# Kernel optimization log

Hardware: AMD Instinct MI355X
Metric: run time of the kernel (lower is better)

Reference implementation:

```python
import jax, jax.numpy as jnp
import numpy as np

# ---- quantization scales (per-tensor, as produced by from_float calibration) ----
IN_SCALE = 0.05      # ForwardTokenizer: fp32 hidden -> int8
ALPHA_Q = 1e-4       # W8A8B8O8 requant multipliers (already include 1/sqrt(head_dim) for q)
ALPHA_K = 1e-4
ALPHA_V = 1e-4
QK_ALPHA = 1e-3      # BMM_S8T_S8N_F32T dequant scale (q_scale * k_scale)
PV_ALPHA = 1.0/127.0 # BMM_S8T_S8N_S8T requant scale ((1/127)*v_scale/out_scale)
OUT_ALPHA = 1e-4     # W8A8BFP32OFP32 dequant scale
NUM_HEADS = 32


def _quant_i8(x, scale):
    # simulate int8 quantization in fp32 (values are exact small integers)
    return jnp.clip(jnp.round(x / scale), -128.0, 127.0)


def _w8a8b8o8(x_i8, W_i8, b_i8, alpha):
    # int8 GEMM with int8 bias, requantized to int8: clamp(round(alpha*(x@W^T) + b))
    acc = jnp.einsum('btd,ed->bte', x_i8, W_i8)  # int32 accumulator in fp32
    return jnp.clip(jnp.round(alpha * acc + b_i8), -128.0, 127.0)


def setup_inputs() -> dict:
    key = jax.random.key(0)
    ks = jax.random.split(key, 10)
    B, T, D = 2, 2048, 2560
    hidden_states = jax.random.normal(ks[0], (B, T, D), dtype=jnp.float32)
    # causal additive mask, shape (B,1,T,T)
    neg = jnp.float32(-1e9)
    causal = jnp.where(jnp.tril(jnp.ones((T, T), dtype=bool)), 0.0, neg)
    attention_mask = jnp.broadcast_to(causal[None, None], (B, 1, T, T)).astype(jnp.float32)
    # int8-valued weights/biases stored as fp32 integers in [-127,127]
    def i8(k, shape):
        return jax.random.randint(k, shape, -127, 128).astype(jnp.float32)
    Wq = i8(ks[1], (D, D)); bq = i8(ks[2], (D,))
    Wk = i8(ks[3], (D, D)); bk = i8(ks[4], (D,))
    Wv = i8(ks[5], (D, D)); bv = i8(ks[6], (D,))
    Wo = i8(ks[7], (D, D))
    bo = jax.random.normal(ks[8], (D,), dtype=jnp.float32) * 0.01  # fp32 out bias
    return {"hidden_states": hidden_states, "attention_mask": attention_mask,
            "Wq": Wq, "bq": bq, "Wk": Wk, "bk": bk, "Wv": Wv, "bv": bv,
            "Wo": Wo, "bo": bo}


def reference(hidden_states, attention_mask, Wq, bq, Wk, bk, Wv, bv, Wo, bo):
    B, T, D = hidden_states.shape
    H = NUM_HEADS
    Dh = D // H
    # ForwardTokenizer: fp32 -> int8
    x_i8 = _quant_i8(hidden_states, IN_SCALE)
    # fused int8 q/k/v projections (W8A8B8O8Linear)
    q = _w8a8b8o8(x_i8, Wq, bq, ALPHA_Q)
    k = _w8a8b8o8(x_i8, Wk, bk, ALPHA_K)
    v = _w8a8b8o8(x_i8, Wv, bv, ALPHA_V)
    # (B,T,D) -> (B,H,T,Dh)
    def shape(t):
        return t.reshape(B, T, H, Dh).transpose(0, 2, 1, 3)
    q, k, v = shape(q), shape(k), shape(v)
    # BMM_S8T_S8N_F32T: int8 q @ k^T dequantized to fp32
    attn_weights = QK_ALPHA * jnp.einsum('bhqd,bhkd->bhqk', q, k)
    attn_weights = attn_weights + attention_mask  # (B,H,T,T)
    attn_weights = jnp.maximum(attn_weights, jnp.finfo(jnp.float32).min)
    attn_probs = jax.nn.softmax(attn_weights, axis=-1)
    # requantize probs to int8: mul_(127).round_()
    p_i8 = jnp.round(attn_probs * 127.0)
    # BMM_S8T_S8N_S8T: int8 p @ v requantized to int8
    attn_out = jnp.clip(jnp.round(PV_ALPHA * jnp.einsum('bhqk,bhkd->bhqd', p_i8, v)), -128.0, 127.0)
    # (B,H,T,Dh) -> (B,T,D)
    attn_out = attn_out.transpose(0, 2, 1, 3).reshape(B, T, D)
    # W8A8BFP32OFP32Linear: int8 GEMM, fp32 dequant + fp32 bias
    out = OUT_ALPHA * jnp.einsum('btd,ed->bte', attn_out, Wo) + bo
    return out
```

## Files before the change

### kernel.cpp

```cpp
#include <hip/hip_runtime.h>
#include <stdint.h>

typedef int v4i __attribute__((ext_vector_type(4)));

#define MFMA_I8(a,b,c) __builtin_amdgcn_mfma_i32_16x16x64_i8(a,b,c,0,0,0)

#define TD 2560
#define TT 2048
#define TB 2
#define TH 32
#define TDH 80
#define TDHP 128
#define TM 4096

#define LOG2E_MS 1.4426950408889634e-3f
#define MASKI (-(1<<30))
#define MAGICF 12582912.0f

__device__ __forceinline__ float clamp8f(float v){ return fminf(fmaxf(v, -128.0f), 127.0f); }
__device__ __forceinline__ float fexp2(float x){ return __builtin_amdgcn_exp2f(x); }

__device__ __forceinline__ void gl_lds16(const int8_t* g, int8_t* l){
  __builtin_amdgcn_global_load_lds(
      (const __attribute__((address_space(1))) void*)g,
      (__attribute__((address_space(3))) void*)l, 16, 0, 0);
}

__global__ void k_quant(const float* __restrict__ x, int8_t* __restrict__ y, int n4){
  int stride = gridDim.x * blockDim.x;
  for (int i = blockIdx.x*blockDim.x + threadIdx.x; i < n4; i += stride){
    float4 v = ((const float4*)x)[i];
    char4 o;
    o.x = (int8_t)clamp8f(rintf(__fdiv_rn(v.x, 0.05f)));
    o.y = (int8_t)clamp8f(rintf(__fdiv_rn(v.y, 0.05f)));
    o.z = (int8_t)clamp8f(rintf(__fdiv_rn(v.z, 0.05f)));
    o.w = (int8_t)clamp8f(rintf(__fdiv_rn(v.w, 0.05f)));
    ((char4*)y)[i] = o;
  }
}

__global__ void k_conv4(const float* __restrict__ w0, const float* __restrict__ w1,
                        const float* __restrict__ w2, const float* __restrict__ w3,
                        int8_t* __restrict__ y0, int8_t* __restrict__ y1,
                        int8_t* __restrict__ y2, int8_t* __restrict__ y3, int n4){
  const int z = blockIdx.y;
  const float* w = z == 0 ? w0 : (z == 1 ? w1 : (z == 2 ? w2 : w3));
  int8_t* y = z == 0 ? y0 : (z == 1 ? y1 : (z == 2 ? y2 : y3));
  int stride = gridDim.x * blockDim.x;
  for (int i = blockIdx.x*blockDim.x + threadIdx.x; i < n4; i += stride){
    float4 v = ((const float4*)w)[i];
    char4 o;
    o.x = (int8_t)(int)rintf(v.x);
    o.y = (int8_t)(int)rintf(v.y);
    o.z = (int8_t)(int)rintf(v.z);
    o.w = (int8_t)(int)rintf(v.w);
    ((char4*)y)[i] = o;
  }
}

#define GB_SETUP                                                     \
  const int t = threadIdx.x;                                         \
  const int wv = t >> 6, l = t & 63, lhi = (l >> 4) & 3, llo = l & 15;\
  const int wr = wv >> 1, wc = wv & 1;                               \
  const int grow = t >> 3;                                           \
  const int gcol = ((t & 7) ^ ((t >> 3) & 7)) * 16;                  \
  const int sc0 = ((lhi ^ (llo & 7)) << 4);

#define GB_KLOOP(xsrc, wsrc)                                         \
  const int8_t* xa = (xsrc) + (size_t)(m0 + grow)*TD + gcol;         \
  const int8_t* wb = (wsrc) + (size_t)(n0 + grow)*TD + gcol;         \
  v4i acc[4][4] = {};                                                \
  for (int k0 = 0; k0 < TD; k0 += 128){                              \
    _Pragma("unroll")                                                \
    for (int i = 0; i < 4; ++i){                                     \
      gl_lds16(xa + (size_t)(i*32)*TD + k0, &As[(i*32 + wv*8)*128]); \
      gl_lds16(wb + (size_t)(i*32)*TD + k0, &Bs[(i*32 + wv*8)*128]); \
    }                                                                \
    __syncthreads();                                                 \
    v4i a[4][2], b[4][2];                                            \
    _Pragma("unroll")                                                \
    for (int mi = 0; mi < 4; ++mi){                                  \
      a[mi][0] = *(const v4i*)&As[(wr*64 + mi*16 + llo)*128 + sc0];  \
      a[mi][1] = *(const v4i*)&As[(wr*64 + mi*16 + llo)*128 + (sc0 ^ 64)];\
    }                                                                \
    _Pragma("unroll")                                                \
    for (int ni = 0; ni < 4; ++ni){                                  \
      b[ni][0] = *(const v4i*)&Bs[(wc*64 + ni*16 + llo)*128 + sc0];  \
      b[ni][1] = *(const v4i*)&Bs[(wc*64 + ni*16 + llo)*128 + (sc0 ^ 64)];\
    }                                                                \
    _Pragma("unroll")                                                \
    for (int mi = 0; mi < 4; ++mi)                                   \
      _Pragma("unroll")                                              \
      for (int ni = 0; ni < 4; ++ni){                                \
        acc[mi][ni] = MFMA_I8(a[mi][0], b[ni][0], acc[mi][ni]);      \
        acc[mi][ni] = MFMA_I8(a[mi][1], b[ni][1], acc[mi][ni]);      \
      }                                                              \
    __syncthreads();                                                 \
  }

__global__ __launch_bounds__(256) void k_qkvg(const int8_t* __restrict__ x,
    const int8_t* __restrict__ w0_, const int8_t* __restrict__ w1_, const int8_t* __restrict__ w2_,
    const float* __restrict__ b0_, const float* __restrict__ b1_, const float* __restrict__ b2_,
    int8_t* __restrict__ dq, int8_t* __restrict__ dk, int8_t* __restrict__ dv)
{
  __shared__ __align__(16) int8_t As[128*128];
  __shared__ __align__(16) int8_t Bs[128*128];
  const int z = blockIdx.z;
  const int8_t* w = z == 0 ? w0_ : (z == 1 ? w1_ : w2_);
  const float* bias = z == 0 ? b0_ : (z == 1 ? b1_ : b2_);
  const int m0 = blockIdx.x * 128, n0 = blockIdx.y * 128;
  GB_SETUP;
  GB_KLOOP(x, w);

  #pragma unroll
  for (int mi = 0; mi < 4; ++mi)
  #pragma unroll
  for (int ni = 0; ni < 4; ++ni)
  #pragma unroll
  for (int r = 0; r < 4; ++r){
    int rowg = m0 + wr*64 + mi*16 + lhi*4 + r;
    int colg = n0 + wc*64 + ni*16 + llo;
    float fv = __fadd_rn(__fmul_rn(1e-4f, (float)acc[mi][ni][r]), bias[colg]);
    int8_t q8 = (int8_t)clamp8f(rintf(fv));
    int bb = rowg >> 11, tl = rowg & 2047;
    int hh = colg / 80, dh = colg - hh*80;
    if (z == 0)      dq[((size_t)(bb*TH + hh)*TT + tl)*TDHP + dh] = q8;
    else if (z == 1) dk[((size_t)(bb*TH + hh)*TT + tl)*TDHP + dh] = q8;
    else             dv[((size_t)(bb*TH + hh)*TDH + dh)*TT + tl] = q8;
  }
}

__global__ __launch_bounds__(256) void k_oproj128(const int8_t* __restrict__ x,
    const int8_t* __restrict__ w, const float* __restrict__ bo,
    float* __restrict__ out)
{
  __shared__ __align__(16) int8_t As[128*128];
  __shared__ __align__(16) int8_t Bs[128*128];
  const int m0 = blockIdx.x * 128, n0 = blockIdx.y * 128;
  GB_SETUP;
  GB_KLOOP(x, w);

  #pragma unroll
  for (int mi = 0; mi < 4; ++mi)
  #pragma unroll
  for (int ni = 0; ni < 4; ++ni)
  #pragma unroll
  for (int r = 0; r < 4; ++r){
    int rowg = m0 + wr*64 + mi*16 + lhi*4 + r;
    int colg = n0 + wc*64 + ni*16 + llo;
    out[(size_t)rowg*TD + colg] =
        __fadd_rn(__fmul_rn(1e-4f, (float)acc[mi][ni][r]), bo[colg]);
  }
}

__global__ __launch_bounds__(256, 6) void k_attn6(const int8_t* __restrict__ qb_,
    const int8_t* __restrict__ kb_, const int8_t* __restrict__ vt_,
    int8_t* __restrict__ ao)
{
  __shared__ __align__(16) int8_t Ks[64*128];
  const int flat = blockIdx.x;
  const int g = flat & 7, ii = flat >> 3;
  const int qt = 31 - (ii >> 3);
  const int pair = g*8 + (ii & 7);
  const int h = pair & 31, b = pair >> 5;

  const int t = threadIdx.x, wv = t >> 6, l = t & 63, lhi = (l >> 4) & 3, llo = l & 15;
  const size_t bh = (size_t)(b*TH + h);
  const int8_t* qb = qb_ + bh*TT*TDHP;
  const int8_t* kb = kb_ + bh*TT*TDHP;
  const int8_t* vb = vt_ + bh*TDH*TT;

  const int qw0 = qt*64 + wv*16;
  const int qg = qw0 + llo;
  const int ktmax = qt + 1;

  int koff0[4], koff1[4];
  #pragma unroll
  for (int sub = 0; sub < 4; ++sub){
    const int row = sub*16 + llo, sw = row & 7;
    koff0[sub] = row*128 + (((lhi  ) ^ sw) << 4);
    koff1[sub] = row*128 + (((lhi+4) ^ sw) << 4);
  }

  v4i qa0 = *(const v4i*)(qb + (size_t)(qw0 + llo)*TDHP + lhi*16);
  v4i qa1 = {0,0,0,0};
  if (lhi == 0) qa1 = *(const v4i*)(qb + (size_t)(qw0 + llo)*TDHP + 64);

  const int srow = t >> 2, scp = (t & 3) * 2, ssw = srow & 7;
  const int8_t* kg = kb + (size_t)srow*TDHP + scp*16;
  int8_t* sdst0 = &Ks[srow*128 + (((scp  ) ^ ssw) << 4)];
  int8_t* sdst1 = &Ks[srow*128 + (((scp+1) ^ ssw) << 4)];

  int   M  = MASKI;
  float cm = __fmul_rn(LOG2E_MS, (float)MASKI);
  float ls = 0.0f;

  v4i pr0 = *(const v4i*)(kg);
  v4i pr1 = *(const v4i*)(kg + 16);
  *(v4i*)sdst0 = pr0; *(v4i*)sdst1 = pr1;
  for (int kt = 0; kt < ktmax; ++kt){
    if (kt + 1 < ktmax){
      pr0 = *(const v4i*)(kg + (size_t)(kt+1)*64*TDHP);
      pr1 = *(const v4i*)(kg + (size_t)(kt+1)*64*TDHP + 16);
    }
    __syncthreads();
    int sv[4][4];
    if (kt < qt){
      #pragma unroll
      for (int sub = 0; sub < 4; ++sub){
        v4i kf0 = *(const v4i*)&Ks[koff0[sub]];
        v4i kf1 = *(const v4i*)&Ks[koff1[sub]];
        v4i d = {}; d = MFMA_I8(kf0, qa0, d); d = MFMA_I8(kf1, qa1, d);
        sv[sub][0]=d[0]; sv[sub][1]=d[1]; sv[sub][2]=d[2]; sv[sub][3]=d[3];
      }
    } else {
      #pragma unroll
      for (int sub = 0; sub < 4; ++sub){
        if (sub <= wv){
          v4i kf0 = *(const v4i*)&Ks[koff0[sub]];
          v4i kf1 = *(const v4i*)&Ks[koff1[sub]];
          v4i d = {}; d = MFMA_I8(kf0, qa0, d); d = MFMA_I8(kf1, qa1, d);
          const int base = kt*64 + sub*16 + lhi*4;
          #pragma unroll
          for (int r = 0; r < 4; ++r)
            sv[sub][r] = (base + r <= qg) ? d[r] : MASKI;
        } else {
          #pragma unroll
          for (int r = 0; r < 4; ++r) sv[sub][r] = MASKI;
        }
      }
    }
    int m0 = max(max(sv[0][0], sv[0][1]), sv[0][2]);
    int m1 = max(max(sv[0][3], sv[1][0]), sv[1][1]);
    int m2 = max(max(sv[1][2], sv[1][3]), sv[2][0]);
    int m3 = max(max(sv[2][1], sv[2][2]), sv[2][3]);
    int m4 = max(max(sv[3][0], sv[3][1]), sv[3][2]);
    int tm = max(max(max(m0, m1), max(m2, m3)), max(m4, sv[3][3]));
    int Mn = max(M, tm);
    float cmN = __fmul_rn(LOG2E_MS, (float)Mn);
    float fac = fexp2(__fsub_rn(cm, cmN));
    float tot = 0.0f;
    #pragma unroll
    for (int sub = 0; sub < 4; ++sub){
      float e0 = fexp2(__fmaf_rn((float)sv[sub][0], LOG2E_MS, -cmN));
      float e1 = fexp2(__fmaf_rn((float)sv[sub][1], LOG2E_MS, -cmN));
      float e2 = fexp2(__fmaf_rn((float)sv[sub][2], LOG2E_MS, -cmN));
      float e3 = fexp2(__fmaf_rn((float)sv[sub][3], LOG2E_MS, -cmN));
      tot = __fadd_rn(tot, __fadd_rn(__fadd_rn(e0, e1), __fadd_rn(e2, e3)));
    }
    ls = __fmaf_rn(ls, fac, tot);
    M = Mn; cm = cmN;
    __syncthreads();
    if (kt + 1 < ktmax){ *(v4i*)sdst0 = pr0; *(v4i*)sdst1 = pr1; }
  }

  float rq;
  {
    float mm = cm, ll = ls;
    #pragma unroll
    for (int off = 16; off < 64; off <<= 1){
      float om = __shfl_xor(mm, off);
      float ol = __shfl_xor(ll, off);
      float mn = fmaxf(mm, om);
      ll = __fadd_rn(__fmul_rn(ll, fexp2(__fsub_rn(mm, mn))),
                     __fmul_rn(ol, fexp2(__fsub_rn(om, mn))));
      mm = mn;
    }
    cm = mm;
    rq = __fdiv_rn(127.0f, ll);
  }

  v4i pacc[5] = {};
  pr0 = *(const v4i*)(kg);
  pr1 = *(const v4i*)(kg + 16);
  __syncthreads();
  *(v4i*)sdst0 = pr0; *(v4i*)sdst1 = pr1;
  for (int kt = 0; kt < ktmax; ++kt){
    if (kt + 1 < ktmax){
      pr0 = *(const v4i*)(kg + (size_t)(kt+1)*64*TDHP);
      pr1 = *(const v4i*)(kg + (size_t)(kt+1)*64*TDHP + 16);
    }
    __syncthreads();
    uint32_t w[4] = {0u,0u,0u,0u};
    if (kt < qt){
      #pragma unroll
      for (int sub = 0; sub < 4; ++sub){
        v4i kf0 = *(const v4i*)&Ks[koff0[sub]];
        v4i kf1 = *(const v4i*)&Ks[koff1[sub]];
        v4i d = {}; d = MFMA_I8(kf0, qa0, d); d = MFMA_I8(kf1, qa1, d);
        uint32_t u0 = __float_as_uint(__fmaf_rn(fexp2(__fmaf_rn((float)d[0], LOG2E_MS, -cm)), rq, MAGICF));
        uint32_t u1 = __float_as_uint(__fmaf_rn(fexp2(__fmaf_rn((float)d[1], LOG2E_MS, -cm)), rq, MAGICF));
        uint32_t u2 = __float_as_uint(__fmaf_rn(fexp2(__fmaf_rn((float)d[2], LOG2E_MS, -cm)), rq, MAGICF));
        uint32_t u3 = __float_as_uint(__fmaf_rn(fexp2(__fmaf_rn((float)d[3], LOG2E_MS, -cm)), rq, MAGICF));
        w[sub] = (u0 & 0xffu) | ((u1 & 0xffu) << 8) | ((u2 & 0xffu) << 16) | (u3 << 24);
      }
    } else {
      #pragma unroll
      for (int sub = 0; sub < 4; ++sub){
        if (sub <= wv){
          v4i kf0 = *(const v4i*)&Ks[koff0[sub]];
          v4i kf1 = *(const v4i*)&Ks[koff1[sub]];
          v4i d = {}; d = MFMA_I8(kf0, qa0, d); d = MFMA_I8(kf1, qa1, d);
          const int base = kt*64 + sub*16 + lhi*4;
          uint32_t wrd = 0u;
          #pragma unroll
          for (int r = 0; r < 4; ++r){
            int sel = (base + r <= qg) ? d[r] : MASKI;
            uint32_t u = __float_as_uint(__fmaf_rn(fexp2(__fmaf_rn((float)sel, LOG2E_MS, -cm)), rq, MAGICF));
            wrd |= (u & 0xffu) << (8*r);
          }
          w[sub] = wrd;
        }
      }
    }
    #pragma unroll
    for (int bb = 0; bb < 2; ++bb){
      const int dist = 16 << bb;
      const int gb = (lhi >> bb) & 1;
      uint32_t nw[4];
      #pragma unroll
      for (int s = 0; s < 4; ++s){
        uint32_t tv = __shfl_xor(w[s ^ (1 << bb)], dist);
        nw[s] = (((s >> bb) & 1) == gb) ? w[s] : tv;
      }
      w[0]=nw[0]; w[1]=nw[1]; w[2]=nw[2]; w[3]=nw[3];
    }
    v4i pa;
    pa[0]=(int)w[0]; pa[1]=(int)w[1]; pa[2]=(int)w[2]; pa[3]=(int)w[3];
    #pragma unroll
    for (int dt = 0; dt < 5; ++dt){
      v4i vf = *(const v4i*)(vb + (size_t)(dt*16 + llo)*TT + kt*64 + lhi*16);
      pacc[dt] = MFMA_I8(vf, pa, pacc[dt]);
    }
    __syncthreads();
    if (kt + 1 < ktmax){ *(v4i*)sdst0 = pr0; *(v4i*)sdst1 = pr1; }
  }

  #pragma unroll
  for (int dt = 0; dt < 5; ++dt){
    uint32_t ob = 0u;
    #pragma unroll
    for (int r = 0; r < 4; ++r){
      int vq = (int)clamp8f(rintf(__fmul_rn((float)pacc[dt][r], (float)(1.0/127.0))));
      ob |= ((uint32_t)(uint8_t)(int8_t)vq) << (8*r);
    }
    *(uint32_t*)(ao + ((size_t)(b*TT) + qw0 + llo)*TD + h*TDH + dt*16 + lhi*4) = ob;
  }
}

extern "C" void kernel_launch(void* const* d_in, const int* in_sizes, int n_in,
                              void* d_out, int out_size, void* d_ws, size_t ws_size,
                              hipStream_t stream) {
  const float* hidden = (const float*)d_in[0];
  const float* Wq = (const float*)d_in[2];
  const float* bq = (const float*)d_in[3];
  const float* Wk = (const float*)d_in[4];
  const float* bk = (const float*)d_in[5];
  const float* Wv = (const float*)d_in[6];
  const float* bv = (const float*)d_in[7];
  const float* Wo = (const float*)d_in[8];
  const float* bo = (const float*)d_in[9];
  float* out = (float*)d_out;

  char* ws = (char*)d_ws;
  const size_t SZ_X  = (size_t)TM * TD;
  const size_t SZ_W  = (size_t)TD * TD;
  const size_t SZ_QK = (size_t)TB * TH * TT * TDHP;
  const size_t SZ_V  = (size_t)TB * TH * TDH * TT;
  int8_t* x8   = (int8_t*)ws;
  int8_t* wq8  = (int8_t*)(ws + SZ_X);
  int8_t* wk8  = wq8 + SZ_W;
  int8_t* wv8  = wk8 + SZ_W;
  int8_t* wo8  = wv8 + SZ_W;
  int8_t* qpad = wo8 + SZ_W;
  int8_t* kpad = qpad + SZ_QK;
  int8_t* vt   = kpad + SZ_QK;
  int8_t* ao   = vt + SZ_V;

  k_quant<<<4096, 256, 0, stream>>>(hidden, x8, (int)(SZ_X/4));
  k_conv4<<<dim3(1024, 4), 256, 0, stream>>>(Wq, Wk, Wv, Wo, wq8, wk8, wv8, wo8, (int)(SZ_W/4));

  k_qkvg<<<dim3(TM/128, TD/128, 3), 256, 0, stream>>>(x8, wq8, wk8, wv8, bq, bk, bv,
                                                      qpad, kpad, vt);

  k_attn6<<<dim3(2048), 256, 0, stream>>>(qpad, kpad, vt, ao);

  k_oproj128<<<dim3(TM/128, TD/128), 256, 0, stream>>>(ao, wo8, bo, out);
}
```

Before: 317.9 us.

## Double-buffer output projection GEMM with async LDS loads and K=64 stages

Replaces the shared GB_KLOOP in the output projection kernel with a custom double-buffered loop. It uses 64-wide K tiles and two LDS buffers, so the global-to-LDS loads for the next tile overlap the MFMA work on the current one. LDS footprint stays the same, and launch bounds now request 4 blocks per CU. The cost is more barriers per K step and hand-coded vmcnt waits, which are fragile if the load count changes.

```diff
diff --git a/kernel.cpp b/kernel.cpp
--- a/kernel.cpp
+++ b/kernel.cpp
@@ -130,15 +130,65 @@
   }
 }
 
-__global__ __launch_bounds__(256) void k_oproj128(const int8_t* __restrict__ x,
+#define OP_STAGE(bufi, k0) do{                                      \
+    gl_lds16(xa0 + (k0), &As[bufi][(wv*16)*64]);                    \
+    gl_lds16(xa1 + (k0), &As[bufi][(64 + wv*16)*64]);               \
+    gl_lds16(wb0 + (k0), &Bs[bufi][(wv*16)*64]);                    \
+    gl_lds16(wb1 + (k0), &Bs[bufi][(64 + wv*16)*64]); }while(0)
+
+#define OP_COMP(bufi) do{                                           \
+    v4i a[4], b[4];                                                 \
+    _Pragma("unroll")                                               \
+    for (int mi = 0; mi < 4; ++mi)                                  \
+      a[mi] = *(const v4i*)&As[bufi][(wr*64 + mi*16 + llo)*64 + sca];\
+    _Pragma("unroll")                                               \
+    for (int ni = 0; ni < 4; ++ni)                                  \
+      b[ni] = *(const v4i*)&Bs[bufi][(wc*64 + ni*16 + llo)*64 + sca];\
+    _Pragma("unroll")                                               \
+    for (int mi = 0; mi < 4; ++mi)                                  \
+      _Pragma("unroll")                                             \
+      for (int ni = 0; ni < 4; ++ni)                                \
+        acc[mi][ni] = MFMA_I8(a[mi], b[ni], acc[mi][ni]); }while(0)
+
+__global__ __launch_bounds__(256, 4) void k_oproj128(const int8_t* __restrict__ x,
     const int8_t* __restrict__ w, const float* __restrict__ bo,
     float* __restrict__ out)
 {
-  __shared__ __align__(16) int8_t As[128*128];
-  __shared__ __align__(16) int8_t Bs[128*128];
+  __shared__ __align__(16) int8_t As[2][128*64];
+  __shared__ __align__(16) int8_t Bs[2][128*64];
   const int m0 = blockIdx.x * 128, n0 = blockIdx.y * 128;
-  GB_SETUP;
-  GB_KLOOP(x, w);
+  const int t = threadIdx.x;
+  const int wv = t >> 6, l = t & 63, lhi = (l >> 4) & 3, llo = l & 15;
+  const int wr = wv >> 1, wc = wv & 1;
+  const int grow = l >> 2;
+  const int gcol = ((l & 3) ^ ((l >> 3) & 3)) * 16;
+
+  const int8_t* xa0 = x + (size_t)(m0 + wv*16 + grow)*TD + gcol;
+  const int8_t* xa1 = x + (size_t)(m0 + 64 + wv*16 + grow)*TD + gcol;
+  const int8_t* wb0 = w + (size_t)(n0 + wv*16 + grow)*TD + gcol;
+  const int8_t* wb1 = w + (size_t)(n0 + 64 + wv*16 + grow)*TD + gcol;
+
+  const int sca = (lhi ^ ((llo >> 1) & 3)) << 4;
+
+  v4i acc[4][4] = {};
+  OP_STAGE(0, 0);
+  #pragma unroll 1
+  for (int p = 0; p < 20; ++p){
+    OP_STAGE(1, (2*p+1)*64);
+    asm volatile("s_waitcnt vmcnt(4)" ::: "memory");
+    __builtin_amdgcn_s_barrier();
+    OP_COMP(0);
+    __builtin_amdgcn_s_barrier();
+    if (p < 19){
+      OP_STAGE(0, (2*p+2)*64);
+      asm volatile("s_waitcnt vmcnt(4)" ::: "memory");
+    } else {
+      asm volatile("s_waitcnt vmcnt(0)" ::: "memory");
+    }
+    __builtin_amdgcn_s_barrier();
+    OP_COMP(1);
+    __builtin_amdgcn_s_barrier();
+  }
 
   #pragma unroll
   for (int mi = 0; mi < 4; ++mi)
```

After: 308.4 us. 3.0% less time.
